# Kernel optimization log

Measured on AMD Instinct MI355X. Metric: run time of the kernel, lower is better.

Reference implementation:

```python
import jax, jax.numpy as jnp
import numpy as np

HIDDEN = 128
N_RBF = 32
LMAX = 2
N_NODES = 10000
DEG = 8  # each node has DEG outgoing (and DEG incoming) edges on a ring


def _build_graph():
    src = np.repeat(np.arange(N_NODES, dtype=np.int64), DEG)
    offs = np.tile(np.arange(1, DEG + 1, dtype=np.int64), N_NODES)
    dst = (src + offs) % N_NODES
    keys = src * N_NODES + dst
    order = np.argsort(keys)
    src2, dst2 = src[order], dst[order]  # e2 sorted by key (searchsorted invariant)
    e1_to_e2 = np.empty_like(order)
    e1_to_e2[order] = np.arange(order.size)
    return src, dst, src2, dst2, e1_to_e2


def setup_inputs() -> dict:
    key = jax.random.key(0)
    ks = jax.random.split(key, 12)
    src1, dst1, src2, dst2, e1_to_e2 = _build_graph()
    E1, E2 = src1.size, src2.size
    in_dim = 6 * HIDDEN + 3 * N_RBF + 1  # 865

    def lin(k, fi, fo):
        kw, kb = jax.random.split(k)
        s = 1.0 / np.sqrt(fi)
        return (jax.random.uniform(kw, (fi, fo), minval=-s, maxval=s),
                jax.random.uniform(kb, (fo,), minval=-s, maxval=s))

    w1, b1 = lin(ks[0], in_dim, HIDDEN)
    w2, b2 = lin(ks[1], HIDDEN, HIDDEN)
    wgw, bgw = lin(ks[2], HIDDEN, HIDDEN)
    wgt, bgt = lin(ks[3], HIDDEN, HIDDEN)
    return {
        "t_e2": jax.random.normal(ks[4], (E2, HIDDEN), dtype=jnp.float32),
        "h": jax.random.normal(ks[5], (N_NODES, HIDDEN), dtype=jnp.float32),
        "edge_index1": jnp.asarray(np.stack([src1, dst1])),
        "edge_index2": jnp.asarray(np.stack([src2, dst2])),
        "e1_to_e2": jnp.asarray(e1_to_e2),
        "dist_e1": jax.random.uniform(ks[6], (E1,), dtype=jnp.float32),
        "dist_e2": jax.random.uniform(ks[7], (E2,), dtype=jnp.float32),
        "rbf_e1": jax.random.normal(ks[8], (E1, N_RBF), dtype=jnp.float32),
        "rbf_e2": jax.random.normal(ks[9], (E2, N_RBF), dtype=jnp.float32),
        "sph_e1": jax.random.normal(ks[10], (E1, LMAX + 1), dtype=jnp.float32),
        "num_nodes": N_NODES,
        "w1": w1, "b1": b1, "w2": w2, "b2": b2,
        "wgw": wgw, "bgw": bgw, "wgt": wgt, "bgt": bgt,
    }


def _wedge_indices(edge_index1, edge_index2, num_nodes):
    """Host-side (numpy, vectorized) wedge construction: for every center node k,
    all (incoming edge i->k, outgoing edge k->j) pairs with i != j, kept only when
    (i, j) itself is an edge in e2 (looked up by sorted key search)."""
    src1 = np.asarray(edge_index1[0]); dst1 = np.asarray(edge_index1[1])
    src2 = np.asarray(edge_index2[0]); dst2 = np.asarray(edge_index2[1])
    nz = src1 != dst1  # drop self-loops
    s, d = src1[nz], dst1[nz]
    eid = np.nonzero(nz)[0]
    out_deg = np.bincount(s, minlength=num_nodes)
    out_order = np.argsort(s, kind="stable")  # filtered-edge positions grouped by src
    out_ptr = np.concatenate([np.zeros(1, np.int64), np.cumsum(out_deg)])
    reps = out_deg[d]  # each incoming edge pairs with out_deg[center] outgoing edges
    total = int(reps.sum())
    if total == 0:
        z = np.zeros(0, np.int64)
        return z, z, z, z, z, z
    starts = np.cumsum(reps) - reps
    local = np.arange(total) - np.repeat(starts, reps)
    kj_f = out_order[np.repeat(out_ptr[d], reps) + local]
    i = np.repeat(s, reps)
    k = np.repeat(d, reps)
    eik = np.repeat(eid, reps)
    j = d[kj_f]
    ekj = eid[kj_f]
    m = i != j
    i, k, j, eik, ekj = i[m], k[m], j[m], eik[m], ekj[m]
    e2_keys = src2.astype(np.int64) * num_nodes + dst2
    pk = i.astype(np.int64) * num_nodes + j
    pos = np.searchsorted(e2_keys, pk)
    posc = np.minimum(pos, e2_keys.size - 1)
    valid = (pos < e2_keys.size) & (e2_keys[posc] == pk)
    return i[valid], k[valid], j[valid], eik[valid], ekj[valid], posc[valid]


def reference(t_e2, h, edge_index1, edge_index2, e1_to_e2, dist_e1, dist_e2,
              rbf_e1, rbf_e2, sph_e1, num_nodes,
              w1, b1, w2, b2, wgw, bgw, wgt, bgt):
    i, k, j, eik, ekj, eij = _wedge_indices(edge_index1, edge_index2, int(num_nodes))
    if i.size == 0:
        return t_e2
    i, k, j = jnp.asarray(i), jnp.asarray(k), jnp.asarray(j)
    eik, ekj, eij = jnp.asarray(eik), jnp.asarray(ekj), jnp.asarray(eij)
    e1e2 = jnp.asarray(e1_to_e2)
    # wedge geometric features (wedge_use_high_degree=False -> l=1 contraction only)
    c_feat = (sph_e1[eik, 1] * sph_e1[ekj, 1])[:, None]           # [W, 1]
    g = jnp.concatenate([rbf_e1[eik], rbf_e1[ekj], rbf_e2[eij], c_feat], axis=-1)
    rho_in = jnp.concatenate([t_e2[e1e2[eik]], t_e2[e1e2[ekj]], t_e2[eij],
                              h[i], h[k], h[j], g], axis=-1)       # [W, 865]
    msg = jax.nn.silu(rho_in @ w1 + b1) @ w2 + b2                  # [W, H]
    m = jax.ops.segment_sum(msg, eij, num_segments=t_e2.shape[0])  # [E2, H]
    return t_e2 + jax.nn.sigmoid(m @ wgw + bgw) * jnp.tanh(t_e2 @ wgt + bgt)
```

## Files before the change

### kernel.cpp

```cpp
#include <hip/hip_runtime.h>
#include <math.h>

typedef unsigned short u16;
typedef unsigned int u32;
typedef __bf16 bf16x8 __attribute__((ext_vector_type(8)));
typedef float f32x4 __attribute__((ext_vector_type(4)));

__device__ __forceinline__ float bf2f(u16 v){ union{u32 u;float f;}c; c.u=((u32)v)<<16; return c.f; }
__device__ __forceinline__ u16 f2bf(float f){ union{__bf16 h; u16 u;}c; c.h=(__bf16)f; return c.u; }
__device__ __forceinline__ u32 pk2(float a, float b){
  union{ __bf16 h[2]; u32 u; }c; c.h[0]=(__bf16)a; c.h[1]=(__bf16)b; return c.u;
}
__device__ __forceinline__ uint4 ld8f(const float* p){
  float4 x = ((const float4*)p)[0];
  float4 y = ((const float4*)p)[1];
  uint4 r; r.x=pk2(x.x,x.y); r.y=pk2(x.z,x.w); r.z=pk2(y.x,y.y); r.w=pk2(y.z,y.w);
  return r;
}
__device__ __forceinline__ float fsilu(float x){
  return x*__builtin_amdgcn_rcpf(1.f+__expf(-x));
}

__global__ void k_setup_all(const int* __restrict__ e1_to_e2,
                            const float* __restrict__ rbf_e1,
                            const float* __restrict__ sph_e1,
                            u16* __restrict__ rbf1p, float* __restrict__ sph_c, int E1,
                            const int* __restrict__ src2, int* __restrict__ out_ptr,
                            int Nn, int E2,
                            const float* __restrict__ w1, u16* __restrict__ Wall,
                            const float* __restrict__ w2, const float* __restrict__ wgw,
                            const float* __restrict__ wgt, const float* __restrict__ b2,
                            u16* __restrict__ WcT, u16* __restrict__ WgtT,
                            float* __restrict__ bc2,
                            int nb0, int nb1, int nb2) {
  const int b = blockIdx.x, t = threadIdx.x;
  if (b < nb0) {
    int e = b*256 + t;
    if (e >= E1) return;
    int f = e1_to_e2[e];
    sph_c[f] = sph_e1[e*3+1];
    const float* s = rbf_e1 + (size_t)e*32;
    uint4* d = (uint4*)(rbf1p + (size_t)f*32);
    d[0]=ld8f(s); d[1]=ld8f(s+8); d[2]=ld8f(s+16); d[3]=ld8f(s+24);
  } else if (b < nb1) {
    int n = (b-nb0)*256 + t;
    if (n > Nn) return;
    int lo=0, hi=E2;
    while (lo<hi){ int m=(lo+hi)>>1; if (src2[m]<n) lo=m+1; else hi=m; }
    out_ptr[n]=lo;
  } else if (b < nb2) {
    int id = (b-nb1)*256 + t;
    if (id < 61440) {
      int m = id / 20480;
      int r2 = id - m*20480;
      int n = r2 / 160, k = r2 - n*160;
      int row;
      if (m==0)      row = (k<128)? k       : 768+(k-128);
      else if (m==1) row = (k<128)? 128+k   : 800+(k-128);
      else           row = (k<128)? 256+k   : 832+(k-128);
      Wall[id] = f2bf(w1[row*128+n]);
    } else if (id < 110592) {
      int idh = id - 61440;
      int m = idh >> 14;
      int r2 = idh & 16383;
      int n = r2 >> 7, k = r2 & 127;
      int base = 384 + m*128;
      Wall[id] = f2bf(w1[(base+k)*128+n]);
    }
  } else {
    int id = (b-nb2)*256 + t;
    if (id < 16384) {
      int n = id&127, k = id>>7;
      float s = 0.f;
      for (int r=0;r<128;r++) s += w2[k*128+r]*wgw[r*128+n];
      WcT[n*128+k] = f2bf(s);
      WgtT[n*128+k] = f2bf(wgt[k*128+n]);
    } else if (id < 16384+128) {
      int n = id-16384;
      float s = 0.f;
      for (int r=0;r<128;r++) s += b2[r]*wgw[r*128+n];
      bc2[n] = s;
    }
  }
}

__global__ __launch_bounds__(256, 2)
void k_gemmH(const float* __restrict__ h, const u16* __restrict__ WH,
             u16* __restrict__ Hout, int Nn) {
  const int bm = blockIdx.x, bn = blockIdx.y;
  const u16* Bp = WH + bn*16384;
  u16* dst = Hout + (size_t)bn*Nn*128;
  __shared__ u16 As[128*40];
  __shared__ u16 Bs[128*40];
  const int tid = threadIdx.x;
  const int lane = tid & 63, wave = tid >> 6;
  const int wm = wave >> 1, wn = wave & 1;
  const int quad = lane >> 4, l16 = lane & 15;
  const int part = tid & 3;
  const int ra = tid >> 2;
  const int rb = ra + 64;
  long fa = (long)bm*128 + ra; if (fa >= Nn) fa = Nn-1;
  long fb = (long)bm*128 + rb; if (fb >= Nn) fb = Nn-1;

  f32x4 acc[4][4] = {};
  for (int ks=0; ks<4; ks++) {
    const int kb = ks*32;
    uint4 va = ld8f(h + fa*128 + kb + part*8);
    uint4 vb = ld8f(h + fb*128 + kb + part*8);
    uint4 wa = *(const uint4*)(Bp + (long)ra*128 + kb + part*8);
    uint4 wb = *(const uint4*)(Bp + (long)rb*128 + kb + part*8);
    __syncthreads();
    *(uint4*)(As + ra*40 + part*8) = va;
    *(uint4*)(As + rb*40 + part*8) = vb;
    *(uint4*)(Bs + ra*40 + part*8) = wa;
    *(uint4*)(Bs + rb*40 + part*8) = wb;
    __syncthreads();
    bf16x8 af[4], bfr[4];
    #pragma unroll
    for (int t=0;t<4;t++) {
      af[t]  = *(const bf16x8*)(As + (wm*64 + t*16 + l16)*40 + quad*8);
      bfr[t] = *(const bf16x8*)(Bs + (wn*64 + t*16 + l16)*40 + quad*8);
    }
    #pragma unroll
    for (int tm=0;tm<4;tm++)
      #pragma unroll
      for (int tn=0;tn<4;tn++)
        acc[tm][tn] = __builtin_amdgcn_mfma_f32_16x16x32_bf16(af[tm], bfr[tn], acc[tm][tn], 0,0,0);
  }
  #pragma unroll
  for (int tm=0;tm<4;tm++) {
    const int rloc = wm*64 + tm*16 + quad*4;
    #pragma unroll
    for (int r=0;r<4;r++) {
      long row = (long)bm*128 + rloc + r;
      if (row >= Nn) continue;
      #pragma unroll
      for (int tn=0;tn<4;tn++) {
        const int col = wn*64 + tn*16 + l16;
        dst[row*128 + col] = f2bf(acc[tm][tn][r]);
      }
    }
  }
}

__global__ __launch_bounds__(256, 8)
void k_wedge(const int* __restrict__ src2, const int* __restrict__ dst2,
             const int* __restrict__ out_ptr, const float* __restrict__ sph_c,
             const u16* __restrict__ Q1, const u16* __restrict__ Q2,
             const u16* __restrict__ P3, const float* __restrict__ w1,
             u16* __restrict__ S, int* __restrict__ cnt, int E2) {
  int gw = (int)((blockIdx.x*256 + threadIdx.x) >> 6);
  int lane = threadIdx.x & 63;
  if (gw >= E2) return;
  int i = src2[gw], j = dst2[gw];
  int f = 0, lo = 0; float cf = 0.f; bool valid = false;
  if (lane < 8) {
    int ff = out_ptr[i] + lane;
    if (ff < out_ptr[i+1]) {
      int k = dst2[ff];
      int l = out_ptr[k], hh = out_ptr[k+1], h0 = hh;
      while (l<hh){ int m=(l+hh)>>1; if (dst2[m]<j) l=m+1; else hh=m; }
      if (l<h0 && dst2[l]==j){ valid=true; f=ff; lo=l; cf=sph_c[ff]*sph_c[l]; }
    }
  }
  unsigned long long mask = __ballot(valid);
  const int nw = __popcll(mask);
  if (lane==0) cnt[gw] = nw;
  u32 p3u = ((const u32*)(P3 + (size_t)gw*128))[lane];
  float p30 = bf2f((u16)(p3u&0xffff)), p31 = bf2f((u16)(p3u>>16));
  float2 wv = ((const float2*)(w1 + 864*128))[lane];
  const u32* q1b = (const u32*)Q1;
  const u32* q2b = (const u32*)Q2;

  u32 xa[8], ya[8]; float ca[8];
  unsigned long long m2 = mask;
  #pragma unroll
  for (int s=0; s<8; s++) {
    if (s < nw) {
      int b = __ffsll((long long)m2)-1; m2 &= m2-1;
      int fA = __builtin_amdgcn_readlane(f, b);
      int lA = __builtin_amdgcn_readlane(lo, b);
      ca[s] = __int_as_float(__builtin_amdgcn_readlane(__float_as_int(cf), b));
      xa[s] = q1b[((size_t)(u32)fA<<6) + lane];
      ya[s] = q2b[((size_t)(u32)lA<<6) + lane];
    }
  }

  float a0=0.f, a1=0.f;
  #pragma unroll
  for (int s=0; s<8; s++) {
    if (s < nw) {
      float b0 = fmaf(ca[s], wv.x, p30);
      float b1 = fmaf(ca[s], wv.y, p31);
      float x0 = b0 + bf2f((u16)(xa[s]&0xffff)) + bf2f((u16)(ya[s]&0xffff));
      float x1 = b1 + bf2f((u16)(xa[s]>>16))    + bf2f((u16)(ya[s]>>16));
      a0 += fsilu(x0);
      a1 += fsilu(x1);
    }
  }
  ((u32*)(S + (size_t)gw*128))[lane] = pk2(a0, a1);
}

struct GArgs {
  const float* t_f32; const float* rbf_e2;
  const u16* rbf1p; const u16* Asrc;
  const int* src2; const int* dst2; const int* cnt;
  const u16* B0; const u16* B1; const u16* B2;
  const u16* Hi; const u16* Hk; const u16* Hj;
  const u16* Bmat; const u16* Bmat2;
  const float* b1; const float* bgw; const float* bgt; const float* bc2;
  u16* out0; u16* out1; u16* out2;
  float* outf;
  int M;
};

__global__ __launch_bounds__(256, 2)
void k_gemm0(GArgs a) {
  const int nwg = gridDim.x;
  const int id  = blockIdx.x;
  const int xcd = id & 7, idx = id >> 3;
  const int q = nwg >> 3, r = nwg & 7;
  const int w = (xcd < r ? xcd*(q+1) : r*(q+1) + (xcd-r)*q) + idx;
  const int bm = w/3, bn = w - bm*3;

  __shared__ u16 sm[32768];
  u16* As = sm;
  u16* Bs = sm + 5120;
  const int tid = threadIdx.x;
  const int lane = tid & 63, wave = tid >> 6;
  const int wm = wave >> 1, wn = wave & 1;
  const int quad = lane >> 4, l16 = lane & 15;

  const int part = tid & 3;
  const int ra = tid >> 2;
  const int rb = ra + 64;
  long fa = (long)bm*128 + ra;
  long fb = (long)bm*128 + rb;
  if (fa >= a.M) fa = a.M-1;
  if (fb >= a.M) fb = a.M-1;

  const u16* Bp = (bn==0)? a.B0 : (bn==1)? a.B1 : a.B2;
  constexpr int KT = 160;

  f32x4 acc[4][4] = {};
  for (int ks=0; ks<5; ks++) {
    const int kb = ks*32;
    uint4 va, vb;
    if (ks<4)        { va = ld8f(a.t_f32 + fa*128 + kb + part*8);
                       vb = ld8f(a.t_f32 + fb*128 + kb + part*8); }
    else if (bn<2)   { va = *(const uint4*)(a.rbf1p + fa*32 + part*8);
                       vb = *(const uint4*)(a.rbf1p + fb*32 + part*8); }
    else             { va = ld8f(a.rbf_e2 + fa*32 + part*8);
                       vb = ld8f(a.rbf_e2 + fb*32 + part*8); }
    uint4 wa = *(const uint4*)(Bp + (long)ra*KT + kb + part*8);
    uint4 wb = *(const uint4*)(Bp + (long)rb*KT + kb + part*8);
    __syncthreads();
    *(uint4*)(As + ra*40 + part*8) = va;
    *(uint4*)(As + rb*40 + part*8) = vb;
    *(uint4*)(Bs + ra*40 + part*8) = wa;
    *(uint4*)(Bs + rb*40 + part*8) = wb;
    __syncthreads();
    bf16x8 af[4], bfr[4];
    #pragma unroll
    for (int t=0;t<4;t++) {
      af[t]  = *(const bf16x8*)(As + (wm*64 + t*16 + l16)*40 + quad*8);
      bfr[t] = *(const bf16x8*)(Bs + (wn*64 + t*16 + l16)*40 + quad*8);
    }
    #pragma unroll
    for (int tm=0;tm<4;tm++)
      #pragma unroll
      for (int tn=0;tn<4;tn++)
        acc[tm][tn] = __builtin_amdgcn_mfma_f32_16x16x32_bf16(af[tm], bfr[tn], acc[tm][tn], 0,0,0);
  }

  if (bn < 2) {
    __syncthreads();
    #pragma unroll
    for (int c=0;c<8;c++) {
      int idx2 = tid + c*256;
      int row = idx2 >> 4, ch = idx2 & 15;
      long fr = (long)bm*128 + row;
      if (fr >= a.M) fr = a.M-1;
      if (bn==0) {
        int s = a.src2[fr], d = a.dst2[fr];
        *(uint4*)(&sm[row*128 + ch*8])         = *(const uint4*)(a.Hi + (long)s*128 + ch*8);
        *(uint4*)(&sm[16384 + row*128 + ch*8]) = *(const uint4*)(a.Hk + (long)d*128 + ch*8);
      } else {
        int d = a.dst2[fr];
        *(uint4*)(&sm[row*128 + ch*8])         = *(const uint4*)(a.Hj + (long)d*128 + ch*8);
      }
    }
    __syncthreads();
  }

  u16* dst = (bn==0)? a.out0 : (bn==1)? a.out1 : a.out2;
  #pragma unroll
  for (int tm=0;tm<4;tm++) {
    const int rloc = wm*64 + tm*16 + quad*4;
    #pragma unroll
    for (int r=0;r<4;r++) {
      long row = (long)bm*128 + rloc + r;
      if (row >= a.M) continue;
      const int rl = rloc + r;
      #pragma unroll
      for (int tn=0;tn<4;tn++) {
        const int col = wn*64 + tn*16 + l16;
        float v = acc[tm][tn][r];
        if (bn==0)      v += bf2f(sm[rl*128+col]) + bf2f(sm[16384+rl*128+col]);
        else if (bn==1) v += bf2f(sm[rl*128+col]);
        else            v += a.b1[col];
        dst[row*128 + col] = f2bf(v);
      }
    }
  }
}

__global__ __launch_bounds__(256, 2)
void k_gemm12(GArgs a) {
  __shared__ u16 As[128*40];
  __shared__ u16 Bs[128*40];
  const int tid = threadIdx.x;
  const int bm = blockIdx.x;
  const int lane = tid & 63, wave = tid >> 6;
  const int wm = wave >> 1, wn = wave & 1;
  const int quad = lane >> 4, l16 = lane & 15;

  const int part = tid & 3;
  const int ra = tid >> 2;
  const int rb = ra + 64;
  long fa = (long)bm*128 + ra;
  long fb = (long)bm*128 + rb;
  if (fa >= a.M) fa = a.M-1;
  if (fb >= a.M) fb = a.M-1;

  f32x4 acc1[4][4] = {};
  f32x4 acc2[4][4] = {};
  for (int ks=0; ks<4; ks++) {
    const int kb = ks*32;
    uint4 va = *(const uint4*)(a.Asrc + fa*128 + kb + part*8);
    uint4 vb = *(const uint4*)(a.Asrc + fb*128 + kb + part*8);
    uint4 wa = *(const uint4*)(a.Bmat + (long)ra*128 + kb + part*8);
    uint4 wbv= *(const uint4*)(a.Bmat + (long)rb*128 + kb + part*8);
    __syncthreads();
    *(uint4*)(As + ra*40 + part*8) = va;
    *(uint4*)(As + rb*40 + part*8) = vb;
    *(uint4*)(Bs + ra*40 + part*8) = wa;
    *(uint4*)(Bs + rb*40 + part*8) = wbv;
    __syncthreads();
    bf16x8 af[4], bfr[4];
    #pragma unroll
    for (int t=0;t<4;t++) {
      af[t]  = *(const bf16x8*)(As + (wm*64 + t*16 + l16)*40 + quad*8);
      bfr[t] = *(const bf16x8*)(Bs + (wn*64 + t*16 + l16)*40 + quad*8);
    }
    #pragma unroll
    for (int tm=0;tm<4;tm++)
      #pragma unroll
      for (int tn=0;tn<4;tn++)
        acc1[tm][tn] = __builtin_amdgcn_mfma_f32_16x16x32_bf16(af[tm], bfr[tn], acc1[tm][tn], 0,0,0);
  }
  for (int ks=0; ks<4; ks++) {
    const int kb = ks*32;
    uint4 va = ld8f(a.t_f32 + fa*128 + kb + part*8);
    uint4 vb = ld8f(a.t_f32 + fb*128 + kb + part*8);
    uint4 wa = *(const uint4*)(a.Bmat2 + (long)ra*128 + kb + part*8);
    uint4 wbv= *(const uint4*)(a.Bmat2 + (long)rb*128 + kb + part*8);
    __syncthreads();
    *(uint4*)(As + ra*40 + part*8) = va;
    *(uint4*)(As + rb*40 + part*8) = vb;
    *(uint4*)(Bs + ra*40 + part*8) = wa;
    *(uint4*)(Bs + rb*40 + part*8) = wbv;
    __syncthreads();
    bf16x8 af[4], bfr[4];
    #pragma unroll
    for (int t=0;t<4;t++) {
      af[t]  = *(const bf16x8*)(As + (wm*64 + t*16 + l16)*40 + quad*8);
      bfr[t] = *(const bf16x8*)(Bs + (wn*64 + t*16 + l16)*40 + quad*8);
    }
    #pragma unroll
    for (int tm=0;tm<4;tm++)
      #pragma unroll
      for (int tn=0;tn<4;tn++)
        acc2[tm][tn] = __builtin_amdgcn_mfma_f32_16x16x32_bf16(af[tm], bfr[tn], acc2[tm][tn], 0,0,0);
  }

  #pragma unroll
  for (int tm=0;tm<4;tm++) {
    const int rloc = wm*64 + tm*16 + quad*4;
    #pragma unroll
    for (int r=0;r<4;r++) {
      long row = (long)bm*128 + rloc + r;
      if (row >= a.M) continue;
      #pragma unroll
      for (int tn=0;tn<4;tn++) {
        const int col = wn*64 + tn*16 + l16;
        float u = acc1[tm][tn][r] + (float)a.cnt[row]*a.bc2[col] + a.bgw[col];
        float g = __builtin_amdgcn_rcpf(1.f+__expf(-u));
        float vv = acc2[tm][tn][r] + a.bgt[col];
        float th = 1.f - 2.f*__builtin_amdgcn_rcpf(__expf(2.f*vv)+1.f);
        float t  = a.t_f32[row*128+col];
        a.outf[row*128+col] = t + g*th;
      }
    }
  }
}

extern "C" void kernel_launch(void* const* d_in, const int* in_sizes, int n_in,
                              void* d_out, int out_size, void* d_ws, size_t ws_size,
                              hipStream_t stream) {
  const float* t_e2  = (const float*)d_in[0];
  const float* h     = (const float*)d_in[1];
  const int* ei2     = (const int*)d_in[3];
  const int* e1_to_e2 = (const int*)d_in[4];
  const float* rbf_e1 = (const float*)d_in[7];
  const float* rbf_e2 = (const float*)d_in[8];
  const float* sph_e1 = (const float*)d_in[9];
  const float* w1  = (const float*)d_in[11];
  const float* b1  = (const float*)d_in[12];
  const float* w2  = (const float*)d_in[13];
  const float* b2  = (const float*)d_in[14];
  const float* wgw = (const float*)d_in[15];
  const float* bgw = (const float*)d_in[16];
  const float* wgt = (const float*)d_in[17];
  const float* bgt = (const float*)d_in[18];

  const int E2 = in_sizes[0]/128;
  const int Nn = in_sizes[1]/128;
  const int E1 = in_sizes[5];
  const int* src2 = ei2;
  const int* dst2 = ei2 + E2;

  char* p = (char*)d_ws;
  u16* Q1 = (u16*)p;       p += (size_t)E2*128*2;
  u16* Q2 = (u16*)p;       p += (size_t)E2*128*2;
  u16* P3 = (u16*)p;       p += (size_t)E2*128*2;
  u16* rbf1p = (u16*)p;    p += (size_t)E2*32*2;
  u16* Hout  = (u16*)p;    p += (size_t)3*Nn*128*2;
  u16* Wall  = (u16*)p;    p += (size_t)110592*2;
  u16* WcT   = (u16*)p;    p += (size_t)128*128*2;
  u16* WgtT  = (u16*)p;    p += (size_t)128*128*2;
  float* sph_c = (float*)p; p += (size_t)E2*4;
  float* bc2   = (float*)p; p += 512;
  int* out_ptr = (int*)p;   p += (((size_t)(Nn+1)*4 + 63)/64)*64;
  int* cnt     = (int*)p;   p += (size_t)E2*4;
  u16* S = P3;
  u16* Hi = Hout, *Hk = Hout + (size_t)Nn*128, *Hj = Hout + (size_t)2*Nn*128;

  const int nb_edges = (E1+255)/256;
  const int nb_ptr   = (Nn+1+255)/256;
  const int nb_w     = (110592+255)/256;
  const int nb_small = (16512+255)/256;
  const int nb0 = nb_edges;
  const int nb1 = nb0 + nb_ptr;
  const int nb2 = nb1 + nb_w;
  const int nbT = nb2 + nb_small;
  k_setup_all<<<nbT, 256, 0, stream>>>(e1_to_e2, rbf_e1, sph_e1, rbf1p, sph_c, E1,
                                       src2, out_ptr, Nn, E2,
                                       w1, Wall, w2, wgw, wgt, b2,
                                       WcT, WgtT, bc2,
                                       nb0, nb1, nb2);

  const int Mh = (Nn+127)/128;
  k_gemmH<<<dim3(Mh,3), 256, 0, stream>>>(h, Wall + 61440, Hout, Nn);

  const int Mb = (E2+127)/128;
  {
    GArgs a = {};
    a.t_f32=t_e2; a.rbf_e2=rbf_e2; a.rbf1p=rbf1p;
    a.src2=src2; a.dst2=dst2;
    a.B0=Wall; a.B1=Wall+20480; a.B2=Wall+40960;
    a.Hi=Hi; a.Hk=Hk; a.Hj=Hj; a.b1=b1;
    a.out0=Q1; a.out1=Q2; a.out2=P3; a.M=E2;
    k_gemm0<<<Mb*3, 256, 0, stream>>>(a);
  }
  k_wedge<<<(E2+3)/4, 256, 0, stream>>>(src2, dst2, out_ptr, sph_c,
                                        Q1, Q2, P3, w1, S, cnt, E2);
  {
    GArgs a = {};
    a.Asrc=S; a.cnt=cnt; a.Bmat=WcT; a.Bmat2=WgtT;
    a.bgw=bgw; a.bgt=bgt; a.bc2=bc2; a.t_f32=t_e2;
    a.outf=(float*)d_out; a.M=E2;
    k_gemm12<<<Mb, 256, 0, stream>>>(a);
  }
}
```

Measured before the change: 329.4 us.

## Stage GEMM epilogue through small LDS tile and gather node rows directly

The k_gemm0 epilogue used to stage gathered H rows into a 64KB shared buffer and then write output one bf16 per thread. It now writes the accumulator tile to LDS in two 64-column halves, then reads it back as 16-byte vectors, adds the gathered node features straight from global memory, and stores coalesced uint4 rows. This shrinks shared memory from 64KB to 20KB, which should allow higher occupancy, and it replaces scattered 2-byte stores with vector stores. The cost is extra synchronisations, and the accumulator is rounded to bf16 before the feature add, which slightly changes numerics.

```diff
diff --git a/kernel.cpp b/kernel.cpp
--- a/kernel.cpp
+++ b/kernel.cpp
@@ -16,6 +16,14 @@
   float4 y = ((const float4*)p)[1];
   uint4 r; r.x=pk2(x.x,x.y); r.y=pk2(x.z,x.w); r.z=pk2(y.x,y.y); r.w=pk2(y.z,y.w);
   return r;
+}
+__device__ __forceinline__ u32 addpk2(u32 a, u32 b){
+  return pk2(bf2f((u16)(a&0xffff))+bf2f((u16)(b&0xffff)),
+             bf2f((u16)(a>>16))   +bf2f((u16)(b>>16)));
+}
+__device__ __forceinline__ u32 addpk3(u32 a, u32 b, u32 c){
+  return pk2(bf2f((u16)(a&0xffff))+bf2f((u16)(b&0xffff))+bf2f((u16)(c&0xffff)),
+             bf2f((u16)(a>>16))   +bf2f((u16)(b>>16))   +bf2f((u16)(c>>16)));
 }
 __device__ __forceinline__ float fsilu(float x){
   return x*__builtin_amdgcn_rcpf(1.f+__expf(-x));
@@ -223,7 +231,7 @@
   const int w = (xcd < r ? xcd*(q+1) : r*(q+1) + (xcd-r)*q) + idx;
   const int bm = w/3, bn = w - bm*3;
 
-  __shared__ u16 sm[32768];
+  __shared__ u16 sm[10240];
   u16* As = sm;
   u16* Bs = sm + 5120;
   const int tid = threadIdx.x;
@@ -273,43 +281,47 @@
         acc[tm][tn] = __builtin_amdgcn_mfma_f32_16x16x32_bf16(af[tm], bfr[tn], acc[tm][tn], 0,0,0);
   }
 
-  if (bn < 2) {
-    __syncthreads();
-    #pragma unroll
-    for (int c=0;c<8;c++) {
-      int idx2 = tid + c*256;
-      int row = idx2 >> 4, ch = idx2 & 15;
-      long fr = (long)bm*128 + row;
-      if (fr >= a.M) fr = a.M-1;
-      if (bn==0) {
-        int s = a.src2[fr], d = a.dst2[fr];
-        *(uint4*)(&sm[row*128 + ch*8])         = *(const uint4*)(a.Hi + (long)s*128 + ch*8);
-        *(uint4*)(&sm[16384 + row*128 + ch*8]) = *(const uint4*)(a.Hk + (long)d*128 + ch*8);
-      } else {
-        int d = a.dst2[fr];
-        *(uint4*)(&sm[row*128 + ch*8])         = *(const uint4*)(a.Hj + (long)d*128 + ch*8);
-      }
-    }
-    __syncthreads();
-  }
-
   u16* dst = (bn==0)? a.out0 : (bn==1)? a.out1 : a.out2;
   #pragma unroll
-  for (int tm=0;tm<4;tm++) {
-    const int rloc = wm*64 + tm*16 + quad*4;
-    #pragma unroll
-    for (int r=0;r<4;r++) {
-      long row = (long)bm*128 + rloc + r;
-      if (row >= a.M) continue;
-      const int rl = rloc + r;
-      #pragma unroll
-      for (int tn=0;tn<4;tn++) {
-        const int col = wn*64 + tn*16 + l16;
-        float v = acc[tm][tn][r];
-        if (bn==0)      v += bf2f(sm[rl*128+col]) + bf2f(sm[16384+rl*128+col]);
-        else if (bn==1) v += bf2f(sm[rl*128+col]);
-        else            v += a.b1[col];
-        dst[row*128 + col] = f2bf(v);
+  for (int h=0; h<2; h++) {
+    __syncthreads();
+    if (wn == h) {
+      #pragma unroll
+      for (int tm=0;tm<4;tm++) {
+        const int rl = wm*64 + tm*16 + quad*4;
+        #pragma unroll
+        for (int tn=0;tn<4;tn++) {
+          const int cl = tn*16 + l16;
+          #pragma unroll
+          for (int r2=0;r2<4;r2++) {
+            float v = acc[tm][tn][r2];
+            if (bn==2) v += a.b1[h*64 + cl];
+            sm[(rl+r2)*72 + cl] = f2bf(v);
+          }
+        }
+      }
+    }
+    __syncthreads();
+    #pragma unroll
+    for (int ps=0; ps<4; ps++) {
+      int id2 = tid + ps*256;
+      int row = id2 >> 3, ch = id2 & 7;
+      long grow = (long)bm*128 + row;
+      if (grow < a.M) {
+        uint4 v = *(uint4*)(sm + row*72 + ch*8);
+        if (bn==0) {
+          int s2 = a.src2[grow], d2 = a.dst2[grow];
+          uint4 h1 = *(const uint4*)(a.Hi + (size_t)(u32)s2*128 + h*64 + ch*8);
+          uint4 h2 = *(const uint4*)(a.Hk + (size_t)(u32)d2*128 + h*64 + ch*8);
+          v.x = addpk3(v.x, h1.x, h2.x); v.y = addpk3(v.y, h1.y, h2.y);
+          v.z = addpk3(v.z, h1.z, h2.z); v.w = addpk3(v.w, h1.w, h2.w);
+        } else if (bn==1) {
+          int d2 = a.dst2[grow];
+          uint4 h1 = *(const uint4*)(a.Hj + (size_t)(u32)d2*128 + h*64 + ch*8);
+          v.x = addpk2(v.x, h1.x); v.y = addpk2(v.y, h1.y);
+          v.z = addpk2(v.z, h1.z); v.w = addpk2(v.w, h1.w);
+        }
+        *(uint4*)(dst + grow*128 + h*64 + ch*8) = v;
       }
     }
   }
```

Result: faster. 299.1 us (-9.2%).
